# Kernel optimization log

Hardware: AMD Instinct MI355X
Metric: run time of the kernel (lower is better)

## Reference

```python
import jax, jax.numpy as jnp
import numpy as np

STRIDES = (8, 4, 2, 1)
EPS = 1e-12  # F.normalize default eps


def _l2norm(x):
    return x / jnp.maximum(jnp.linalg.norm(x, axis=-1, keepdims=True), EPS)


def _stage(residual, stride, iw, ib, ow, ob, cb):
    B, D, T = residual.shape
    # avg_pool1d(stride, stride)
    zp = residual.reshape(B, D, T // stride, stride).mean(-1) if stride > 1 else residual
    # in_proj: 1x1 conv  [B,D,Ts] -> [B,C,Ts]
    z_e = jnp.einsum('bdt,cd->bct', zp, iw) + ib[None, :, None]
    C = z_e.shape[1]
    enc = z_e.transpose(0, 2, 1).reshape(-1, C)           # (B*Ts, C)
    enc_n = _l2norm(enc)
    cb_n = _l2norm(cb)
    dist = (enc_n ** 2).sum(1, keepdims=True) - 2.0 * enc_n @ cb_n.T + (cb_n ** 2).sum(1)[None, :]
    indices = jnp.argmax(-dist, axis=1).reshape(B, -1)    # (B, Ts)
    z_q = cb[indices].transpose(0, 2, 1)                  # (B, C, Ts) -- unnormalized codebook lookup
    commit = ((z_e - jax.lax.stop_gradient(z_q)) ** 2).mean(axis=(1, 2))
    cbloss = ((z_q - jax.lax.stop_gradient(z_e)) ** 2).mean(axis=(1, 2))
    z_q = z_e + jax.lax.stop_gradient(z_q - z_e)          # straight-through
    z_q_out = jnp.einsum('bct,dc->bdt', z_q, ow) + ob[None, :, None]
    if stride > 1:
        z_q_out = jnp.repeat(z_q_out, stride, axis=-1)
        z_e = jnp.repeat(z_e, stride, axis=-1)
    return z_q_out, commit, cbloss, indices, z_e


def setup_inputs() -> dict:
    key = jax.random.key(0)
    ks = jax.random.split(key, 6)
    return {
        'z': jax.random.normal(ks[0], (16, 512, 4096), dtype=jnp.float32),
        'in_w': jax.random.normal(ks[1], (4, 8, 512), dtype=jnp.float32) * 0.05,
        'in_b': jax.random.normal(ks[2], (4, 8), dtype=jnp.float32) * 0.05,
        'out_w': jax.random.normal(ks[3], (4, 512, 8), dtype=jnp.float32) * 0.05,
        'out_b': jax.random.normal(ks[4], (4, 512), dtype=jnp.float32) * 0.05,
        'codebooks': jax.random.normal(ks[5], (4, 1024, 8), dtype=jnp.float32),
    }


def reference(z, in_w, in_b, out_w, out_b, codebooks):
    z_q = jnp.zeros_like(z)
    residual = z
    commitment_loss = 0.0
    codebook_loss = 0.0
    codes = []
    latents = []
    for i, s in enumerate(STRIDES):
        z_q_i, commit_i, cbloss_i, idx_i, z_e_i = _stage(
            residual, s, in_w[i], in_b[i], out_w[i], out_b[i], codebooks[i])
        z_q = z_q + z_q_i  # mask is all-True in eval with n_quantizers = n_codebooks
        residual = residual - z_q_i
        commitment_loss = commitment_loss + commit_i.mean()
        codebook_loss = codebook_loss + cbloss_i.mean()
        codes.append(idx_i)
        latents.append(z_e_i)
    latents = jnp.concatenate(latents, axis=1)  # [B, N*C, T]
    return (z_q, latents, commitment_loss, codebook_loss,
            codes[0], codes[1], codes[2], codes[3])
```

## Files before the change

kernel.cpp:

```cpp
#include <hip/hip_runtime.h>


constexpr int B = 16, D = 512, T = 4096, C = 8, K = 1024, NS = 4;

constexpr long long OUT_ZQ     = 0;
constexpr long long OUT_LAT    = 33554432LL;
constexpr long long OUT_COMMIT = OUT_LAT + 2097152LL;
constexpr long long OUT_CBL    = OUT_COMMIT + 1;
constexpr long long OUT_CODES0 = OUT_CBL + 1;

__host__ __device__ constexpr long long code_off(int j) {
    return OUT_CODES0 + (j >= 1 ? 8192 : 0) + (j >= 2 ? 16384 : 0) + (j >= 3 ? 32768 : 0);
}

constexpr long long WS_CBREC = 0;
constexpr long long WS_OBS   = 49152;
constexpr long long WS_LOSS  = 49664;
constexpr long long WS_CORR  = 49696;
constexpr long long WS_P0    = 52224;
constexpr long long WS_P1    = WS_P0 + 65536;
constexpr long long WS_P2    = WS_P1 + 131072;
constexpr long long WS_P3    = WS_P2 + 262144;
constexpr long long WS_Q0    = WS_P3 + 524288;
constexpr long long WS_Q1    = WS_Q0 + 65536;
constexpr long long WS_Q2    = WS_Q1 + 131072;
constexpr long long WS_Q3    = WS_Q2 + 262144;
constexpr long long WS_TAB   = WS_Q3 + 524288;

__global__ __launch_bounds__(256) void k_prep(
    const float* __restrict__ in_w, const float* __restrict__ out_w,
    const float* __restrict__ out_b, const float* __restrict__ cb,
    float* __restrict__ ws)
{
    int bid = blockIdx.x;
    int tid = threadIdx.x;

    if (bid < 18) {
        int t = bid * 256 + tid;
        if (t == 0) ws[WS_LOSS] = 0.f;
        if (t < NS * K) {
            const float* c = cb + (long long)t * 8;
            float cv[8];
#pragma unroll
            for (int k = 0; k < 8; k++) cv[k] = c[k];
            float n2 = 0.f;
#pragma unroll
            for (int k = 0; k < 8; k++) n2 += cv[k] * cv[k];
            float den = fmaxf(sqrtf(n2), 1e-12f);
            float cn[8];
#pragma unroll
            for (int k = 0; k < 8; k++) cn[k] = cv[k] / den;
            float cn2 = 0.f;
#pragma unroll
            for (int k = 0; k < 8; k++) cn2 += cn[k] * cn[k];
            float* r = ws + WS_CBREC + (long long)t * 12;
#pragma unroll
            for (int k = 0; k < 8; k++) r[k] = -2.0f * cn[k];
            r[8] = cn2; r[9] = 0.f; r[10] = 0.f; r[11] = 0.f;
        } else if (t < NS * K + D) {
            int d = t - NS * K;
            ws[WS_OBS + d] = out_b[d] + out_b[512 + d] + out_b[1024 + d] + out_b[1536 + d];
        }
        return;
    }

    int gw = (bid - 18) * 4 + (tid >> 6);
    int lane = tid & 63;
    if (gw >= 6 * 72) return;
    int p = gw / 72, idx = gw % 72;
    int i, j;
    if (p == 0) { i = 1; j = 0; }
    else if (p < 3) { i = 2; j = p - 1; }
    else { i = 3; j = p - 3; }

    double acc = 0.0;
    if (idx < 64) {
        int ci = idx >> 3, cc = idx & 7;
        const float* wi = in_w + (long long)(i * 8 + ci) * 512;
        const float* wo = out_w + (long long)j * 4096;
#pragma unroll
        for (int k = 0; k < 8; k++) {
            int d = lane + k * 64;
            acc += (double)wi[d] * (double)wo[d * 8 + cc];
        }
    } else {
        int ci = idx - 64;
        const float* wi = in_w + (long long)(i * 8 + ci) * 512;
        const float* bo = out_b + (long long)j * 512;
#pragma unroll
        for (int k = 0; k < 8; k++) {
            int d = lane + k * 64;
            acc += (double)wi[d] * (double)bo[d];
        }
    }
#pragma unroll
    for (int off = 32; off >= 1; off >>= 1) acc += __shfl_down(acc, off);
    if (lane == 0) ((double*)(ws + WS_CORR))[p * 72 + idx] = acc;
}

__global__ __launch_bounds__(256) void k_prep_c(
    const float* __restrict__ cb, float* __restrict__ ws)
{
    int t = blockIdx.x * 256 + threadIdx.x;
    if (t >= 6 * 1024) return;
    int p = t >> 10, code = t & 1023;
    int j = (p == 0) ? 0 : (p < 3) ? (p - 1) : (p - 3);
    const double* M = (const double*)(ws + WS_CORR) + p * 72;
    const float* q = cb + ((long long)j * K + code) * 8;
    float qv[8];
#pragma unroll
    for (int cc = 0; cc < 8; cc++) qv[cc] = q[cc];
    float* trow = ws + WS_TAB + (long long)t * 8;
#pragma unroll
    for (int c = 0; c < 8; c++) {
        double acc = M[64 + c];
#pragma unroll
        for (int cc = 0; cc < 8; cc++) acc += M[c * 8 + cc] * (double)qv[cc];
        trow[c] = (float)acc;
    }
}

__global__ __launch_bounds__(512) void k_pool_proj(
    const float* __restrict__ z, const float* __restrict__ in_w,
    const float* __restrict__ in_b, float* __restrict__ ws)
{
    __shared__ float smem[512 * 36];

    int tid = threadIdx.x;
    int lane = tid & 63;
    int wv = __builtin_amdgcn_readfirstlane(tid >> 6);
    int b = blockIdx.x;
    int t0 = blockIdx.y * 128;

#pragma unroll
    for (int sc = 0; sc < 32; ++sc)
        smem[tid * 36 + sc] = in_w[sc * 512 + tid];
    __syncthreads();

    const float* zrow = z + ((long long)b * D) * T + t0 + lane * 2;

    float a3[2][8] = {};
    float a2[8]    = {};
    float a1[8]    = {};
    float a0[8]    = {};

#pragma unroll 2
    for (int dd = 0; dd < 64; dd++) {
        int d = wv * 64 + dd;
        float2 v = *(const float2*)(zrow + (long long)d * T);
        const float* wrow = smem + d * 36;
        float w0[8], w1[8], w2[8], w3[8];
        *(float4*)&w0[0] = *(const float4*)(wrow + 0);
        *(float4*)&w0[4] = *(const float4*)(wrow + 4);
        *(float4*)&w1[0] = *(const float4*)(wrow + 8);
        *(float4*)&w1[4] = *(const float4*)(wrow + 12);
        *(float4*)&w2[0] = *(const float4*)(wrow + 16);
        *(float4*)&w2[4] = *(const float4*)(wrow + 20);
        *(float4*)&w3[0] = *(const float4*)(wrow + 24);
        *(float4*)&w3[4] = *(const float4*)(wrow + 28);

        float s2 = v.x + v.y;
#pragma unroll
        for (int c = 0; c < 8; c++) {
            a3[0][c] = fmaf(w3[c], v.x, a3[0][c]);
            a3[1][c] = fmaf(w3[c], v.y, a3[1][c]);
            a2[c]    = fmaf(w2[c], s2, a2[c]);
            a1[c]    = fmaf(w1[c], s2, a1[c]);
            a0[c]    = fmaf(w0[c], s2, a0[c]);
        }
    }

    __syncthreads();

    {
        float (*red)[16][64] = (float (*)[16][64])smem;
#pragma unroll
        for (int pos = 0; pos < 2; pos++)
#pragma unroll
            for (int c = 0; c < 8; c++)
                red[wv][pos * 8 + c][lane] = a3[pos][c];
        __syncthreads();
        for (int o = tid; o < 1024; o += 512) {
            int ln = o & 63, s = o >> 6;
            float sum = 0.f;
#pragma unroll
            for (int w = 0; w < 8; w++) sum += red[w][s][ln];
            int pos = s >> 3, c = s & 7;
            int tp = t0 + ln * 2 + pos;
            ws[WS_P3 + ((long long)b * 4096 + tp) * 8 + c] = sum + in_b[3 * 8 + c];
        }
        __syncthreads();
    }

    {
        float (*red)[24][64] = (float (*)[24][64])smem;
#pragma unroll
        for (int c = 0; c < 8; c++) {
            red[wv][c][lane]      = a2[c];
            red[wv][8 + c][lane]  = a1[c];
            red[wv][16 + c][lane] = a0[c];
        }
        __syncthreads();
        for (int o = tid; o < 1536; o += 512) {
            int ln = o & 63, s = o >> 6;
            if (s < 8) {
                int c = s;
                float sum = 0.f;
#pragma unroll
                for (int w = 0; w < 8; w++) sum += red[w][s][ln];
                int tp = (t0 >> 1) + ln;
                ws[WS_P2 + ((long long)b * 2048 + tp) * 8 + c] = sum * 0.5f + in_b[2 * 8 + c];
            } else if (s < 16) {
                if (ln >= 32) continue;
                int c = s - 8;
                float sum = 0.f;
#pragma unroll
                for (int w = 0; w < 8; w++) sum += red[w][s][2 * ln] + red[w][s][2 * ln + 1];
                int tp = (t0 >> 2) + ln;
                ws[WS_P1 + ((long long)b * 1024 + tp) * 8 + c] = sum * 0.25f + in_b[8 + c];
            } else {
                if (ln >= 16) continue;
                int c = s - 16;
                float sum = 0.f;
#pragma unroll
                for (int w = 0; w < 8; w++)
#pragma unroll
                    for (int k = 0; k < 4; k++) sum += red[w][s][4 * ln + k];
                int tp = (t0 >> 3) + ln;
                ws[WS_P0 + ((long long)b * 512 + tp) * 8 + c] = sum * 0.125f + in_b[c];
            }
        }
    }
}

template <int S>
__global__ __launch_bounds__(512) void k_vq(
    const float* __restrict__ cb, float* __restrict__ ws, float* __restrict__ out)
{
    constexpr int TS = 512 << S;
    constexpr long long PBASE = (S == 0) ? WS_P0 : (S == 1) ? WS_P1 : (S == 2) ? WS_P2 : WS_P3;
    constexpr long long QBASE = (S == 0) ? WS_Q0 : (S == 1) ? WS_Q1 : (S == 2) ? WS_Q2 : WS_Q3;
    constexpr int pbase = (S == 1) ? 0 : (S == 2) ? 1 : 3;
    constexpr float LW = 1.0f / (8.0f * (float)TS * (float)B);

    __shared__ float cbl[12288];
    __shared__ float sb[8][64];
    __shared__ unsigned short si[8][64];
    __shared__ float e_lds[64][8];

    int tid = threadIdx.x;
    int lane = tid & 63;
    int w = __builtin_amdgcn_readfirstlane(tid >> 6);

    {
        const float4* src = (const float4*)(ws + WS_CBREC + (long long)S * K * 12);
        float4* dst = (float4*)cbl;
        for (int o = tid; o < 3072; o += 512) dst[o] = src[o];
    }

    long long v = (long long)blockIdx.x * 64 + lane;
    int b = (int)(v >> (9 + S));
    int tp = (int)(v & (TS - 1));

    float e[8];
    const float* P = ws + PBASE + v * 8;
#pragma unroll
    for (int c = 0; c < 8; c++) e[c] = P[c];

    if (S > 0) {
        double ed[8];
#pragma unroll
        for (int c = 0; c < 8; c++) ed[c] = (double)e[c];
#pragma unroll
        for (int j = 0; j < S; j++) {
            int tj = tp >> (S - j);
            long long vj = ((long long)b << (9 + j)) + tj;
            int cidx = (int)out[code_off(j) + vj];
            const float* trow = ws + WS_TAB + ((long long)(pbase + j) * 1024 + cidx) * 8;
#pragma unroll
            for (int c = 0; c < 8; c++) ed[c] -= (double)trow[c];
        }
#pragma unroll
        for (int c = 0; c < 8; c++) e[c] = (float)ed[c];
    }

    float n2 = 0.f;
#pragma unroll
    for (int c = 0; c < 8; c++) n2 = fmaf(e[c], e[c], n2);
    float den = fmaxf(sqrtf(n2), 1e-12f);
    float inv = 1.0f / den;
    float en[8];
#pragma unroll
    for (int c = 0; c < 8; c++) en[c] = e[c] * inv;

    if (w == 0) {
#pragma unroll
        for (int c = 0; c < 8; c++) e_lds[lane][c] = e[c];
    }

    __syncthreads();

    const float* rec = cbl + w * 128 * 12;
    float best = 3.0e38f;
    int bidx = 0;
    for (int jt = 0; jt < 128; jt++) {
        const float* r = rec + jt * 12;
        float acc = r[8];
#pragma unroll
        for (int c = 0; c < 8; c++) acc = fmaf(r[c], en[c], acc);
        if (acc < best) { best = acc; bidx = jt; }
    }
    sb[w][lane] = best;
    si[w][lane] = (unsigned short)(w * 128 + bidx);
    __syncthreads();

    if (tid < 64) {
        float bd = sb[0][lane];
        int bj = si[0][lane];
#pragma unroll
        for (int ww = 1; ww < 8; ww++) {
            float d2 = sb[ww][lane];
            int j2 = si[ww][lane];
            if (d2 < bd || (d2 == bd && j2 < bj)) { bd = d2; bj = j2; }
        }
        const float* qc = cb + ((long long)S * K + bj) * 8;
        float qv[8];
#pragma unroll
        for (int c = 0; c < 8; c++) qv[c] = qc[c];
        float* qo = ws + QBASE + v * 8;
#pragma unroll
        for (int c = 0; c < 8; c++) qo[c] = qv[c];

        out[code_off(S) + v] = (float)bj;

        float l = 0.f;
#pragma unroll
        for (int c = 0; c < 8; c++) { float dq = e[c] - qv[c]; l = fmaf(dq, dq, l); }
#pragma unroll
        for (int off = 32; off >= 1; off >>= 1) l += __shfl_down(l, off);
        if (lane == 0) atomicAdd(ws + WS_LOSS, l * LW);
    }

    constexpr int SREP = 8 >> S;
    {
        long long v0 = (long long)blockIdx.x * 64;
        int b0 = (int)(v0 >> (9 + S));
        int tp0 = (int)(v0 & (TS - 1));
        long long lat0 = OUT_LAT + ((long long)b0 * 32 + S * 8) * T + (long long)tp0 * SREP;
        for (int o = tid; o < 512 * SREP; o += 512) {
            int c = o / (64 * SREP);
            int r = o & (64 * SREP - 1);
            out[lat0 + (long long)c * T + r] = e_lds[r / SREP][c];
        }
    }
}

__global__ __launch_bounds__(256) void k_zq(
    const float* __restrict__ out_w, const float* __restrict__ ws, float* __restrict__ out)
{
    int tid = threadIdx.x;
    int lane = tid & 63;
    int w = __builtin_amdgcn_readfirstlane(tid >> 6);
    int bid = blockIdx.x;
    int tc   = bid & 3;
    int g    = (bid >> 2) & 63;
    int b    = bid >> 8;
    int t    = tc * 1024 + w * 256 + lane * 4;

    float q0[8], q1[8], q2[2][8], q3[4][8];
    {
        const float* Q = ws + WS_Q0 + ((long long)b * 512 + (t >> 3)) * 8;
#pragma unroll
        for (int c = 0; c < 8; c++) q0[c] = Q[c];
    }
    {
        const float* Q = ws + WS_Q1 + ((long long)b * 1024 + (t >> 2)) * 8;
#pragma unroll
        for (int c = 0; c < 8; c++) q1[c] = Q[c];
    }
    {
        const float* Q = ws + WS_Q2 + ((long long)b * 2048 + (t >> 1)) * 8;
#pragma unroll
        for (int j = 0; j < 2; j++)
#pragma unroll
            for (int c = 0; c < 8; c++) q2[j][c] = Q[j * 8 + c];
    }
    {
        const float* Q = ws + WS_Q3 + ((long long)b * 4096 + t) * 8;
#pragma unroll
        for (int j = 0; j < 4; j++)
#pragma unroll
            for (int c = 0; c < 8; c++) q3[j][c] = Q[j * 8 + c];
    }

#pragma unroll 2
    for (int dl = 0; dl < 8; dl++) {
        int d = g * 8 + dl;
        const float* w0 = out_w + 0 * 4096 + d * 8;
        const float* w1 = out_w + 1 * 4096 + d * 8;
        const float* w2 = out_w + 2 * 4096 + d * 8;
        const float* w3 = out_w + 3 * 4096 + d * 8;

        float acc = ws[WS_OBS + d];
#pragma unroll
        for (int c = 0; c < 8; c++) acc = fmaf(w0[c], q0[c], acc);
#pragma unroll
        for (int c = 0; c < 8; c++) acc = fmaf(w1[c], q1[c], acc);
        float accA = acc, accB = acc;
#pragma unroll
        for (int c = 0; c < 8; c++) {
            accA = fmaf(w2[c], q2[0][c], accA);
            accB = fmaf(w2[c], q2[1][c], accB);
        }
        float r0 = accA, r1 = accA, r2 = accB, r3 = accB;
#pragma unroll
        for (int c = 0; c < 8; c++) {
            r0 = fmaf(w3[c], q3[0][c], r0);
            r1 = fmaf(w3[c], q3[1][c], r1);
            r2 = fmaf(w3[c], q3[2][c], r2);
            r3 = fmaf(w3[c], q3[3][c], r3);
        }
        float* o = out + OUT_ZQ + ((long long)b * 512 + d) * T + t;
        *(float4*)o = make_float4(r0, r1, r2, r3);
    }

    if (bid == 0 && tid == 0) {
        float L = ws[WS_LOSS];
        out[OUT_COMMIT] = L;
        out[OUT_CBL]    = L;
    }
}

extern "C" void kernel_launch(void* const* d_in, const int* in_sizes, int n_in,
                              void* d_out, int out_size, void* d_ws, size_t ws_size,
                              hipStream_t stream)
{
    const float* z     = (const float*)d_in[0];
    const float* in_w  = (const float*)d_in[1];
    const float* in_b  = (const float*)d_in[2];
    const float* out_w = (const float*)d_in[3];
    const float* out_b = (const float*)d_in[4];
    const float* cb    = (const float*)d_in[5];
    float* out = (float*)d_out;
    float* ws  = (float*)d_ws;

    k_prep<<<dim3(126), dim3(256), 0, stream>>>(in_w, out_w, out_b, cb, ws);
    k_prep_c<<<dim3(24), dim3(256), 0, stream>>>(cb, ws);
    k_pool_proj<<<dim3(16, 32), dim3(512), 0, stream>>>(z, in_w, in_b, ws);
    k_vq<0><<<dim3(128), dim3(512), 0, stream>>>(cb, ws, out);
    k_vq<1><<<dim3(256), dim3(512), 0, stream>>>(cb, ws, out);
    k_vq<2><<<dim3(512), dim3(512), 0, stream>>>(cb, ws, out);
    k_vq<3><<<dim3(1024), dim3(512), 0, stream>>>(cb, ws, out);
    k_zq<<<dim3(4096), dim3(256), 0, stream>>>(out_w, ws, out);
}
```

Baseline: 151.1 us.

## Fuse prep kernels into pool/vq launches, process two vectors per thread in VQ

Merges the codebook/correction prep work into extra blocks of the pool-projection kernel and moves the table-building prep into the stage-0 VQ kernel, cutting two launches. Each VQ thread now scores two vectors per codebook record, halving the block count and reusing each LDS record read. It also adds software prefetch of z rows in the pooling loop and float4 latent stores. The cost is more registers per VQ thread and reuse of the codebook LDS buffer for the argmin reduction.

```diff
diff --git a/kernel.cpp b/kernel.cpp
--- a/kernel.cpp
+++ b/kernel.cpp
@@ -27,110 +27,84 @@
 constexpr long long WS_Q3    = WS_Q2 + 262144;
 constexpr long long WS_TAB   = WS_Q3 + 524288;
 
-__global__ __launch_bounds__(256) void k_prep(
-    const float* __restrict__ in_w, const float* __restrict__ out_w,
+__global__ __launch_bounds__(512) void k_pool_prep(
+    const float* __restrict__ z, const float* __restrict__ in_w,
+    const float* __restrict__ in_b, const float* __restrict__ out_w,
     const float* __restrict__ out_b, const float* __restrict__ cb,
     float* __restrict__ ws)
 {
+    __shared__ float smem[512 * 36];
+
     int bid = blockIdx.x;
     int tid = threadIdx.x;
-
-    if (bid < 18) {
-        int t = bid * 256 + tid;
-        if (t == 0) ws[WS_LOSS] = 0.f;
-        if (t < NS * K) {
-            const float* c = cb + (long long)t * 8;
-            float cv[8];
-#pragma unroll
-            for (int k = 0; k < 8; k++) cv[k] = c[k];
-            float n2 = 0.f;
-#pragma unroll
-            for (int k = 0; k < 8; k++) n2 += cv[k] * cv[k];
-            float den = fmaxf(sqrtf(n2), 1e-12f);
-            float cn[8];
-#pragma unroll
-            for (int k = 0; k < 8; k++) cn[k] = cv[k] / den;
-            float cn2 = 0.f;
-#pragma unroll
-            for (int k = 0; k < 8; k++) cn2 += cn[k] * cn[k];
-            float* r = ws + WS_CBREC + (long long)t * 12;
-#pragma unroll
-            for (int k = 0; k < 8; k++) r[k] = -2.0f * cn[k];
-            r[8] = cn2; r[9] = 0.f; r[10] = 0.f; r[11] = 0.f;
-        } else if (t < NS * K + D) {
-            int d = t - NS * K;
-            ws[WS_OBS + d] = out_b[d] + out_b[512 + d] + out_b[1024 + d] + out_b[1536 + d];
+    int lane = tid & 63;
+
+    if (bid >= 512) {
+        if (bid < 521) {
+            int t = (bid - 512) * 512 + tid;
+            if (t == 0) ws[WS_LOSS] = 0.f;
+            if (t < NS * K) {
+                const float* c = cb + (long long)t * 8;
+                float cv[8];
+#pragma unroll
+                for (int k = 0; k < 8; k++) cv[k] = c[k];
+                float n2 = 0.f;
+#pragma unroll
+                for (int k = 0; k < 8; k++) n2 += cv[k] * cv[k];
+                float den = fmaxf(sqrtf(n2), 1e-12f);
+                float cn[8];
+#pragma unroll
+                for (int k = 0; k < 8; k++) cn[k] = cv[k] / den;
+                float cn2 = 0.f;
+#pragma unroll
+                for (int k = 0; k < 8; k++) cn2 += cn[k] * cn[k];
+                float* r = ws + WS_CBREC + (long long)t * 12;
+#pragma unroll
+                for (int k = 0; k < 8; k++) r[k] = -2.0f * cn[k];
+                r[8] = cn2; r[9] = 0.f; r[10] = 0.f; r[11] = 0.f;
+            } else if (t < NS * K + D) {
+                int d = t - NS * K;
+                ws[WS_OBS + d] = out_b[d] + out_b[512 + d] + out_b[1024 + d] + out_b[1536 + d];
+            }
+        } else {
+            int gw = (bid - 521) * 8 + (tid >> 6);
+            if (gw >= 6 * 72) return;
+            int p = gw / 72, idx = gw % 72;
+            int i, j;
+            if (p == 0) { i = 1; j = 0; }
+            else if (p < 3) { i = 2; j = p - 1; }
+            else { i = 3; j = p - 3; }
+
+            double acc = 0.0;
+            if (idx < 64) {
+                int ci = idx >> 3, cc = idx & 7;
+                const float* wi = in_w + (long long)(i * 8 + ci) * 512;
+                const float* wo = out_w + (long long)j * 4096;
+#pragma unroll
+                for (int k = 0; k < 8; k++) {
+                    int d = lane + k * 64;
+                    acc += (double)wi[d] * (double)wo[d * 8 + cc];
+                }
+            } else {
+                int ci = idx - 64;
+                const float* wi = in_w + (long long)(i * 8 + ci) * 512;
+                const float* bo = out_b + (long long)j * 512;
+#pragma unroll
+                for (int k = 0; k < 8; k++) {
+                    int d = lane + k * 64;
+                    acc += (double)wi[d] * (double)bo[d];
+                }
+            }
+#pragma unroll
+            for (int off = 32; off >= 1; off >>= 1) acc += __shfl_down(acc, off);
+            if (lane == 0) ((double*)(ws + WS_CORR))[p * 72 + idx] = acc;
         }
         return;
     }
 
-    int gw = (bid - 18) * 4 + (tid >> 6);
-    int lane = tid & 63;
-    if (gw >= 6 * 72) return;
-    int p = gw / 72, idx = gw % 72;
-    int i, j;
-    if (p == 0) { i = 1; j = 0; }
-    else if (p < 3) { i = 2; j = p - 1; }
-    else { i = 3; j = p - 3; }
-
-    double acc = 0.0;
-    if (idx < 64) {
-        int ci = idx >> 3, cc = idx & 7;
-        const float* wi = in_w + (long long)(i * 8 + ci) * 512;
-        const float* wo = out_w + (long long)j * 4096;
-#pragma unroll
-        for (int k = 0; k < 8; k++) {
-            int d = lane + k * 64;
-            acc += (double)wi[d] * (double)wo[d * 8 + cc];
-        }
-    } else {
-        int ci = idx - 64;
-        const float* wi = in_w + (long long)(i * 8 + ci) * 512;
-        const float* bo = out_b + (long long)j * 512;
-#pragma unroll
-        for (int k = 0; k < 8; k++) {
-            int d = lane + k * 64;
-            acc += (double)wi[d] * (double)bo[d];
-        }
-    }
-#pragma unroll
-    for (int off = 32; off >= 1; off >>= 1) acc += __shfl_down(acc, off);
-    if (lane == 0) ((double*)(ws + WS_CORR))[p * 72 + idx] = acc;
-}
-
-__global__ __launch_bounds__(256) void k_prep_c(
-    const float* __restrict__ cb, float* __restrict__ ws)
-{
-    int t = blockIdx.x * 256 + threadIdx.x;
-    if (t >= 6 * 1024) return;
-    int p = t >> 10, code = t & 1023;
-    int j = (p == 0) ? 0 : (p < 3) ? (p - 1) : (p - 3);
-    const double* M = (const double*)(ws + WS_CORR) + p * 72;
-    const float* q = cb + ((long long)j * K + code) * 8;
-    float qv[8];
-#pragma unroll
-    for (int cc = 0; cc < 8; cc++) qv[cc] = q[cc];
-    float* trow = ws + WS_TAB + (long long)t * 8;
-#pragma unroll
-    for (int c = 0; c < 8; c++) {
-        double acc = M[64 + c];
-#pragma unroll
-        for (int cc = 0; cc < 8; cc++) acc += M[c * 8 + cc] * (double)qv[cc];
-        trow[c] = (float)acc;
-    }
-}
-
-__global__ __launch_bounds__(512) void k_pool_proj(
-    const float* __restrict__ z, const float* __restrict__ in_w,
-    const float* __restrict__ in_b, float* __restrict__ ws)
-{
-    __shared__ float smem[512 * 36];
-
-    int tid = threadIdx.x;
-    int lane = tid & 63;
     int wv = __builtin_amdgcn_readfirstlane(tid >> 6);
-    int b = blockIdx.x;
-    int t0 = blockIdx.y * 128;
+    int b = bid & 15;
+    int t0 = (bid >> 4) * 128;
 
 #pragma unroll
     for (int sc = 0; sc < 32; ++sc)
@@ -144,10 +118,17 @@
     float a1[8]    = {};
     float a0[8]    = {};
 
+    float2 zv0 = *(const float2*)(zrow + (long long)(wv * 64 + 0) * T);
+    float2 zv1 = *(const float2*)(zrow + (long long)(wv * 64 + 1) * T);
+
 #pragma unroll 2
     for (int dd = 0; dd < 64; dd++) {
         int d = wv * 64 + dd;
-        float2 v = *(const float2*)(zrow + (long long)d * T);
+        float2 v = zv0;
+        zv0 = zv1;
+        if (dd < 62)
+            zv1 = *(const float2*)(zrow + (long long)(d + 2) * T);
+
         const float* wrow = smem + d * 36;
         float w0[8], w1[8], w2[8], w3[8];
         *(float4*)&w0[0] = *(const float4*)(wrow + 0);
@@ -244,13 +225,12 @@
     constexpr float LW = 1.0f / (8.0f * (float)TS * (float)B);
 
     __shared__ float cbl[12288];
-    __shared__ float sb[8][64];
-    __shared__ unsigned short si[8][64];
-    __shared__ float e_lds[64][8];
+    __shared__ float e_lds[128][8];
 
     int tid = threadIdx.x;
     int lane = tid & 63;
     int w = __builtin_amdgcn_readfirstlane(tid >> 6);
+    int bid = blockIdx.x;
 
     {
         const float4* src = (const float4*)(ws + WS_CBREC + (long long)S * K * 12);
@@ -258,71 +238,89 @@
         for (int o = tid; o < 3072; o += 512) dst[o] = src[o];
     }
 
-    long long v = (long long)blockIdx.x * 64 + lane;
-    int b = (int)(v >> (9 + S));
-    int tp = (int)(v & (TS - 1));
-
-    float e[8];
-    const float* P = ws + PBASE + v * 8;
-#pragma unroll
-    for (int c = 0; c < 8; c++) e[c] = P[c];
-
-    if (S > 0) {
-        double ed[8];
-#pragma unroll
-        for (int c = 0; c < 8; c++) ed[c] = (double)e[c];
-#pragma unroll
-        for (int j = 0; j < S; j++) {
-            int tj = tp >> (S - j);
-            long long vj = ((long long)b << (9 + j)) + tj;
-            int cidx = (int)out[code_off(j) + vj];
-            const float* trow = ws + WS_TAB + ((long long)(pbase + j) * 1024 + cidx) * 8;
-#pragma unroll
-            for (int c = 0; c < 8; c++) ed[c] -= (double)trow[c];
-        }
-#pragma unroll
-        for (int c = 0; c < 8; c++) e[c] = (float)ed[c];
-    }
-
-    float n2 = 0.f;
-#pragma unroll
-    for (int c = 0; c < 8; c++) n2 = fmaf(e[c], e[c], n2);
-    float den = fmaxf(sqrtf(n2), 1e-12f);
-    float inv = 1.0f / den;
-    float en[8];
-#pragma unroll
-    for (int c = 0; c < 8; c++) en[c] = e[c] * inv;
-
-    if (w == 0) {
-#pragma unroll
-        for (int c = 0; c < 8; c++) e_lds[lane][c] = e[c];
+    float enA[8], enB[8];
+    {
+        long long vv[2] = { (long long)bid * 128 + lane, (long long)bid * 128 + 64 + lane };
+#pragma unroll
+        for (int h = 0; h < 2; h++) {
+            long long v = vv[h];
+            int b = (int)(v >> (9 + S));
+            int tp = (int)(v & (TS - 1));
+            float e[8];
+            const float* P = ws + PBASE + v * 8;
+#pragma unroll
+            for (int c = 0; c < 8; c++) e[c] = P[c];
+            if (S > 0) {
+                double ed[8];
+#pragma unroll
+                for (int c = 0; c < 8; c++) ed[c] = (double)e[c];
+#pragma unroll
+                for (int j = 0; j < S; j++) {
+                    int tj = tp >> (S - j);
+                    long long vj = ((long long)b << (9 + j)) + tj;
+                    int cidx = (int)out[code_off(j) + vj];
+                    const float* trow = ws + WS_TAB + ((long long)(pbase + j) * 1024 + cidx) * 8;
+#pragma unroll
+                    for (int c = 0; c < 8; c++) ed[c] -= (double)trow[c];
+                }
+#pragma unroll
+                for (int c = 0; c < 8; c++) e[c] = (float)ed[c];
+            }
+            float n2 = 0.f;
+#pragma unroll
+            for (int c = 0; c < 8; c++) n2 = fmaf(e[c], e[c], n2);
+            float den = fmaxf(sqrtf(n2), 1e-12f);
+            float inv = 1.0f / den;
+            float* en = h ? enB : enA;
+#pragma unroll
+            for (int c = 0; c < 8; c++) en[c] = e[c] * inv;
+            if (w == 0) {
+#pragma unroll
+                for (int c = 0; c < 8; c++) e_lds[h * 64 + lane][c] = e[c];
+            }
+        }
     }
 
     __syncthreads();
 
     const float* rec = cbl + w * 128 * 12;
-    float best = 3.0e38f;
-    int bidx = 0;
+    float bestA = 3.0e38f, bestB = 3.0e38f;
+    int idxA = 0, idxB = 0;
+#pragma unroll 2
     for (int jt = 0; jt < 128; jt++) {
         const float* r = rec + jt * 12;
-        float acc = r[8];
-#pragma unroll
-        for (int c = 0; c < 8; c++) acc = fmaf(r[c], en[c], acc);
-        if (acc < best) { best = acc; bidx = jt; }
-    }
-    sb[w][lane] = best;
-    si[w][lane] = (unsigned short)(w * 128 + bidx);
+        float aA = r[8], aB = r[8];
+#pragma unroll
+        for (int c = 0; c < 8; c++) {
+            float rc = r[c];
+            aA = fmaf(rc, enA[c], aA);
+            aB = fmaf(rc, enB[c], aB);
+        }
+        if (aA < bestA) { bestA = aA; idxA = jt; }
+        if (aB < bestB) { bestB = aB; idxB = jt; }
+    }
+
     __syncthreads();
 
-    if (tid < 64) {
-        float bd = sb[0][lane];
-        int bj = si[0][lane];
+    float* sb_f = cbl;
+    unsigned short* si_u = (unsigned short*)(cbl + 1024);
+    sb_f[w * 128 + lane]      = bestA;
+    sb_f[w * 128 + 64 + lane] = bestB;
+    si_u[w * 128 + lane]      = (unsigned short)(w * 128 + idxA);
+    si_u[w * 128 + 64 + lane] = (unsigned short)(w * 128 + idxB);
+    __syncthreads();
+
+    if (tid < 128) {
+        int sv = tid;
+        float bd = sb_f[sv];
+        int bj = si_u[sv];
 #pragma unroll
         for (int ww = 1; ww < 8; ww++) {
-            float d2 = sb[ww][lane];
-            int j2 = si[ww][lane];
+            float d2 = sb_f[ww * 128 + sv];
+            int j2 = si_u[ww * 128 + sv];
             if (d2 < bd || (d2 == bd && j2 < bj)) { bd = d2; bj = j2; }
         }
+        long long v = (long long)bid * 128 + sv;
         const float* qc = cb + ((long long)S * K + bj) * 8;
         float qv[8];
 #pragma unroll
@@ -335,22 +333,50 @@
 
         float l = 0.f;
 #pragma unroll
-        for (int c = 0; c < 8; c++) { float dq = e[c] - qv[c]; l = fmaf(dq, dq, l); }
+        for (int c = 0; c < 8; c++) { float dq = e_lds[sv][c] - qv[c]; l = fmaf(dq, dq, l); }
 #pragma unroll
         for (int off = 32; off >= 1; off >>= 1) l += __shfl_down(l, off);
-        if (lane == 0) atomicAdd(ws + WS_LOSS, l * LW);
+        if ((tid & 63) == 0) atomicAdd(ws + WS_LOSS, l * LW);
     }
 
     constexpr int SREP = 8 >> S;
-    {
-        long long v0 = (long long)blockIdx.x * 64;
+    constexpr int SH = 3 - S;
+    {
+        long long v0 = (long long)bid * 128;
         int b0 = (int)(v0 >> (9 + S));
         int tp0 = (int)(v0 & (TS - 1));
         long long lat0 = OUT_LAT + ((long long)b0 * 32 + S * 8) * T + (long long)tp0 * SREP;
-        for (int o = tid; o < 512 * SREP; o += 512) {
-            int c = o / (64 * SREP);
-            int r = o & (64 * SREP - 1);
-            out[lat0 + (long long)c * T + r] = e_lds[r / SREP][c];
+        for (int o = tid; o < 256 * SREP; o += 512) {
+            int c = o / (32 * SREP);
+            int i4 = o % (32 * SREP);
+            int r0 = i4 * 4;
+            float4 vv = make_float4(
+                e_lds[(r0 + 0) >> SH][c], e_lds[(r0 + 1) >> SH][c],
+                e_lds[(r0 + 2) >> SH][c], e_lds[(r0 + 3) >> SH][c]);
+            *(float4*)(out + lat0 + (long long)c * T + r0) = vv;
+        }
+    }
+
+    if constexpr (S == 0) {
+        if (bid < 12) {
+            int t = bid * 512 + tid;
+            if (t < 6 * 1024) {
+                int p = t >> 10, code = t & 1023;
+                int j = (p == 0) ? 0 : (p < 3) ? (p - 1) : (p - 3);
+                const double* M = (const double*)(ws + WS_CORR) + p * 72;
+                const float* q = cb + ((long long)j * K + code) * 8;
+                float qvv[8];
+#pragma unroll
+                for (int cc = 0; cc < 8; cc++) qvv[cc] = q[cc];
+                float* trow = ws + WS_TAB + (long long)t * 8;
+#pragma unroll
+                for (int c = 0; c < 8; c++) {
+                    double acc = M[64 + c];
+#pragma unroll
+                    for (int cc = 0; cc < 8; cc++) acc += M[c * 8 + cc] * (double)qvv[cc];
+                    trow[c] = (float)acc;
+                }
+            }
         }
     }
 }
@@ -444,12 +470,10 @@
     float* out = (float*)d_out;
     float* ws  = (float*)d_ws;
 
-    k_prep<<<dim3(126), dim3(256), 0, stream>>>(in_w, out_w, out_b, cb, ws);
-    k_prep_c<<<dim3(24), dim3(256), 0, stream>>>(cb, ws);
-    k_pool_proj<<<dim3(16, 32), dim3(512), 0, stream>>>(z, in_w, in_b, ws);
-    k_vq<0><<<dim3(128), dim3(512), 0, stream>>>(cb, ws, out);
-    k_vq<1><<<dim3(256), dim3(512), 0, stream>>>(cb, ws, out);
-    k_vq<2><<<dim3(512), dim3(512), 0, stream>>>(cb, ws, out);
-    k_vq<3><<<dim3(1024), dim3(512), 0, stream>>>(cb, ws, out);
+    k_pool_prep<<<dim3(575), dim3(512), 0, stream>>>(z, in_w, in_b, out_w, out_b, cb, ws);
+    k_vq<0><<<dim3(64),  dim3(512), 0, stream>>>(cb, ws, out);
+    k_vq<1><<<dim3(128), dim3(512), 0, stream>>>(cb, ws, out);
+    k_vq<2><<<dim3(256), dim3(512), 0, stream>>>(cb, ws, out);
+    k_vq<3><<<dim3(512), dim3(512), 0, stream>>>(cb, ws, out);
     k_zq<<<dim3(4096), dim3(256), 0, stream>>>(out_w, ws, out);
 }
```

After: 169.3 us. 1.12x slower.

## Register-block VQ search over four vectors, widen pool tiles, fold prep_c into pool

Applied to the files above, without the earlier changes.

Each VQ thread now scores four encoder vectors per codebook entry, so every loaded codebook row is reused four times. The codebook is stored as a packed 8-float record plus a separate norm array, and latents are written as float4. The pooling/projection kernel handles 256 time steps per block with float4 loads. The k_prep_c table computation becomes an extra grid row of k_pool_proj, which removes one launch. The trade-off is fewer VQ blocks (as few as 32 for stage 0) and higher register pressure, which may leave the GPU underfilled.

```diff
diff --git a/kernel.cpp b/kernel.cpp
--- a/kernel.cpp
+++ b/kernel.cpp
@@ -14,10 +14,11 @@
 }
 
 constexpr long long WS_CBREC = 0;
-constexpr long long WS_OBS   = 49152;
-constexpr long long WS_LOSS  = 49664;
-constexpr long long WS_CORR  = 49696;
-constexpr long long WS_P0    = 52224;
+constexpr long long WS_CN2   = 32768;
+constexpr long long WS_OBS   = 36864;
+constexpr long long WS_LOSS  = 37376;
+constexpr long long WS_CORR  = 37384;
+constexpr long long WS_P0    = 40960;
 constexpr long long WS_P1    = WS_P0 + 65536;
 constexpr long long WS_P2    = WS_P1 + 131072;
 constexpr long long WS_P3    = WS_P2 + 262144;
@@ -52,11 +53,11 @@
             for (int k = 0; k < 8; k++) cn[k] = cv[k] / den;
             float cn2 = 0.f;
 #pragma unroll
-            for (int k = 0; k < 8; k++) cn2 += cn[k] * cn[k];
-            float* r = ws + WS_CBREC + (long long)t * 12;
+            for (int k = 0; k < 8; k++) cn2 = fmaf(cn[k], cn[k], cn2);
+            float* r = ws + WS_CBREC + (long long)t * 8;
 #pragma unroll
             for (int k = 0; k < 8; k++) r[k] = -2.0f * cn[k];
-            r[8] = cn2; r[9] = 0.f; r[10] = 0.f; r[11] = 0.f;
+            ws[WS_CN2 + t] = cn2;
         } else if (t < NS * K + D) {
             int d = t - NS * K;
             ws[WS_OBS + d] = out_b[d] + out_b[512 + d] + out_b[1024 + d] + out_b[1536 + d];
@@ -98,56 +99,58 @@
     if (lane == 0) ((double*)(ws + WS_CORR))[p * 72 + idx] = acc;
 }
 
-__global__ __launch_bounds__(256) void k_prep_c(
-    const float* __restrict__ cb, float* __restrict__ ws)
-{
-    int t = blockIdx.x * 256 + threadIdx.x;
-    if (t >= 6 * 1024) return;
-    int p = t >> 10, code = t & 1023;
-    int j = (p == 0) ? 0 : (p < 3) ? (p - 1) : (p - 3);
-    const double* M = (const double*)(ws + WS_CORR) + p * 72;
-    const float* q = cb + ((long long)j * K + code) * 8;
-    float qv[8];
-#pragma unroll
-    for (int cc = 0; cc < 8; cc++) qv[cc] = q[cc];
-    float* trow = ws + WS_TAB + (long long)t * 8;
-#pragma unroll
-    for (int c = 0; c < 8; c++) {
-        double acc = M[64 + c];
-#pragma unroll
-        for (int cc = 0; cc < 8; cc++) acc += M[c * 8 + cc] * (double)qv[cc];
-        trow[c] = (float)acc;
-    }
-}
-
 __global__ __launch_bounds__(512) void k_pool_proj(
     const float* __restrict__ z, const float* __restrict__ in_w,
-    const float* __restrict__ in_b, float* __restrict__ ws)
+    const float* __restrict__ in_b, const float* __restrict__ cb,
+    float* __restrict__ ws)
 {
     __shared__ float smem[512 * 36];
 
     int tid = threadIdx.x;
     int lane = tid & 63;
+
+    if (blockIdx.y == 16) {
+        int t = blockIdx.x * 512 + tid;
+        if (t < 6 * 1024) {
+            int p = t >> 10, code = t & 1023;
+            int j = (p == 0) ? 0 : (p < 3) ? (p - 1) : (p - 3);
+            const double* M = (const double*)(ws + WS_CORR) + p * 72;
+            const float* q = cb + ((long long)j * K + code) * 8;
+            float qv[8];
+#pragma unroll
+            for (int cc = 0; cc < 8; cc++) qv[cc] = q[cc];
+            float* trow = ws + WS_TAB + (long long)t * 8;
+#pragma unroll
+            for (int c = 0; c < 8; c++) {
+                double acc = M[64 + c];
+#pragma unroll
+                for (int cc = 0; cc < 8; cc++) acc += M[c * 8 + cc] * (double)qv[cc];
+                trow[c] = (float)acc;
+            }
+        }
+        return;
+    }
+
     int wv = __builtin_amdgcn_readfirstlane(tid >> 6);
     int b = blockIdx.x;
-    int t0 = blockIdx.y * 128;
+    int t0 = blockIdx.y * 256;
 
 #pragma unroll
     for (int sc = 0; sc < 32; ++sc)
         smem[tid * 36 + sc] = in_w[sc * 512 + tid];
     __syncthreads();
 
-    const float* zrow = z + ((long long)b * D) * T + t0 + lane * 2;
-
-    float a3[2][8] = {};
-    float a2[8]    = {};
+    const float* zrow = z + ((long long)b * D) * T + t0 + lane * 4;
+
+    float a3[4][8] = {};
+    float a2[2][8] = {};
     float a1[8]    = {};
     float a0[8]    = {};
 
 #pragma unroll 2
     for (int dd = 0; dd < 64; dd++) {
         int d = wv * 64 + dd;
-        float2 v = *(const float2*)(zrow + (long long)d * T);
+        float4 v = *(const float4*)(zrow + (long long)d * T);
         const float* wrow = smem + d * 36;
         float w0[8], w1[8], w2[8], w3[8];
         *(float4*)&w0[0] = *(const float4*)(wrow + 0);
@@ -159,74 +162,79 @@
         *(float4*)&w3[0] = *(const float4*)(wrow + 24);
         *(float4*)&w3[4] = *(const float4*)(wrow + 28);
 
-        float s2 = v.x + v.y;
+        float s2a = v.x + v.y, s2b = v.z + v.w;
+        float s4 = s2a + s2b;
 #pragma unroll
         for (int c = 0; c < 8; c++) {
             a3[0][c] = fmaf(w3[c], v.x, a3[0][c]);
             a3[1][c] = fmaf(w3[c], v.y, a3[1][c]);
-            a2[c]    = fmaf(w2[c], s2, a2[c]);
-            a1[c]    = fmaf(w1[c], s2, a1[c]);
-            a0[c]    = fmaf(w0[c], s2, a0[c]);
+            a3[2][c] = fmaf(w3[c], v.z, a3[2][c]);
+            a3[3][c] = fmaf(w3[c], v.w, a3[3][c]);
+            a2[0][c] = fmaf(w2[c], s2a, a2[0][c]);
+            a2[1][c] = fmaf(w2[c], s2b, a2[1][c]);
+            a1[c]    = fmaf(w1[c], s4, a1[c]);
+            a0[c]    = fmaf(w0[c], s4, a0[c]);
         }
     }
 
     __syncthreads();
 
     {
-        float (*red)[16][64] = (float (*)[16][64])smem;
-#pragma unroll
-        for (int pos = 0; pos < 2; pos++)
+        float (*red)[32][64] = (float (*)[32][64])smem;
+#pragma unroll
+        for (int pos = 0; pos < 4; pos++)
 #pragma unroll
             for (int c = 0; c < 8; c++)
                 red[wv][pos * 8 + c][lane] = a3[pos][c];
         __syncthreads();
-        for (int o = tid; o < 1024; o += 512) {
+        for (int o = tid; o < 2048; o += 512) {
             int ln = o & 63, s = o >> 6;
             float sum = 0.f;
 #pragma unroll
             for (int w = 0; w < 8; w++) sum += red[w][s][ln];
             int pos = s >> 3, c = s & 7;
-            int tp = t0 + ln * 2 + pos;
+            int tp = t0 + ln * 4 + pos;
             ws[WS_P3 + ((long long)b * 4096 + tp) * 8 + c] = sum + in_b[3 * 8 + c];
         }
         __syncthreads();
     }
 
     {
-        float (*red)[24][64] = (float (*)[24][64])smem;
+        float (*red)[32][64] = (float (*)[32][64])smem;
+#pragma unroll
+        for (int pos = 0; pos < 2; pos++)
+#pragma unroll
+            for (int c = 0; c < 8; c++)
+                red[wv][pos * 8 + c][lane] = a2[pos][c];
 #pragma unroll
         for (int c = 0; c < 8; c++) {
-            red[wv][c][lane]      = a2[c];
-            red[wv][8 + c][lane]  = a1[c];
-            red[wv][16 + c][lane] = a0[c];
+            red[wv][16 + c][lane] = a1[c];
+            red[wv][24 + c][lane] = a0[c];
         }
         __syncthreads();
-        for (int o = tid; o < 1536; o += 512) {
+        for (int o = tid; o < 2048; o += 512) {
             int ln = o & 63, s = o >> 6;
-            if (s < 8) {
-                int c = s;
+            if (s < 16) {
                 float sum = 0.f;
 #pragma unroll
                 for (int w = 0; w < 8; w++) sum += red[w][s][ln];
-                int tp = (t0 >> 1) + ln;
+                int pos = s >> 3, c = s & 7;
+                int tp = (t0 >> 1) + ln * 2 + pos;
                 ws[WS_P2 + ((long long)b * 2048 + tp) * 8 + c] = sum * 0.5f + in_b[2 * 8 + c];
-            } else if (s < 16) {
-                if (ln >= 32) continue;
-                int c = s - 8;
+            } else if (s < 24) {
+                int c = s - 16;
                 float sum = 0.f;
 #pragma unroll
-                for (int w = 0; w < 8; w++) sum += red[w][s][2 * ln] + red[w][s][2 * ln + 1];
+                for (int w = 0; w < 8; w++) sum += red[w][s][ln];
                 int tp = (t0 >> 2) + ln;
                 ws[WS_P1 + ((long long)b * 1024 + tp) * 8 + c] = sum * 0.25f + in_b[8 + c];
             } else {
-                if (ln >= 16) continue;
-                int c = s - 16;
+                if (ln & 1) continue;
+                int c = s - 24;
                 float sum = 0.f;
 #pragma unroll
-                for (int w = 0; w < 8; w++)
-#pragma unroll
-                    for (int k = 0; k < 4; k++) sum += red[w][s][4 * ln + k];
-                int tp = (t0 >> 3) + ln;
+                for (int w = 0; w < 8; w++) sum += red[w][s][ln] + red[w][s][ln + 1];
+                int tp = (t0 >> 3) + (ln >> 1);
                 ws[WS_P0 + ((long long)b * 512 + tp) * 8 + c] = sum * 0.125f + in_b[c];
             }
         }
@@ -243,86 +251,120 @@
     constexpr int pbase = (S == 1) ? 0 : (S == 2) ? 1 : 3;
     constexpr float LW = 1.0f / (8.0f * (float)TS * (float)B);
 
-    __shared__ float cbl[12288];
-    __shared__ float sb[8][64];
-    __shared__ unsigned short si[8][64];
-    __shared__ float e_lds[64][8];
+    __shared__ float recl[1024 * 8];
+    __shared__ float cn2l[1024];
+    __shared__ float e_lds[256][8];
+    __shared__ float sbl[8][256];
+    __shared__ unsigned short sil[8][256];
 
     int tid = threadIdx.x;
     int lane = tid & 63;
     int w = __builtin_amdgcn_readfirstlane(tid >> 6);
-
-    {
-        const float4* src = (const float4*)(ws + WS_CBREC + (long long)S * K * 12);
-        float4* dst = (float4*)cbl;
-        for (int o = tid; o < 3072; o += 512) dst[o] = src[o];
-    }
-
-    long long v = (long long)blockIdx.x * 64 + lane;
-    int b = (int)(v >> (9 + S));
-    int tp = (int)(v & (TS - 1));
-
-    float e[8];
-    const float* P = ws + PBASE + v * 8;
-#pragma unroll
-    for (int c = 0; c < 8; c++) e[c] = P[c];
-
-    if (S > 0) {
-        double ed[8];
-#pragma unroll
-        for (int c = 0; c < 8; c++) ed[c] = (double)e[c];
-#pragma unroll
-        for (int j = 0; j < S; j++) {
-            int tj = tp >> (S - j);
-            long long vj = ((long long)b << (9 + j)) + tj;
-            int cidx = (int)out[code_off(j) + vj];
-            const float* trow = ws + WS_TAB + ((long long)(pbase + j) * 1024 + cidx) * 8;
-#pragma unroll
-            for (int c = 0; c < 8; c++) ed[c] -= (double)trow[c];
-        }
-#pragma unroll
-        for (int c = 0; c < 8; c++) e[c] = (float)ed[c];
-    }
-
-    float n2 = 0.f;
-#pragma unroll
-    for (int c = 0; c < 8; c++) n2 = fmaf(e[c], e[c], n2);
-    float den = fmaxf(sqrtf(n2), 1e-12f);
-    float inv = 1.0f / den;
-    float en[8];
-#pragma unroll
-    for (int c = 0; c < 8; c++) en[c] = e[c] * inv;
-
-    if (w == 0) {
-#pragma unroll
-        for (int c = 0; c < 8; c++) e_lds[lane][c] = e[c];
+    int bid = blockIdx.x;
+
+    {
+        const float4* rs = (const float4*)(ws + WS_CBREC + (long long)S * 8192);
+        float4* rd = (float4*)recl;
+        for (int o = tid; o < 2048; o += 512) rd[o] = rs[o];
+        const float4* cs = (const float4*)(ws + WS_CN2 + (long long)S * 1024);
+        float4* cd = (float4*)cn2l;
+        for (int o = tid; o < 256; o += 512) cd[o] = cs[o];
+    }
+
+    float en[4][8];
+#pragma unroll
+    for (int h = 0; h < 4; h++) {
+        int sv = h * 64 + lane;
+        long long v = (long long)bid * 256 + sv;
+        int b = (int)(v >> (9 + S));
+        int tp = (int)(v & (TS - 1));
+
+        float e[8];
+        const float* P = ws + PBASE + v * 8;
+#pragma unroll
+        for (int c = 0; c < 8; c++) e[c] = P[c];
+
+        if constexpr (S > 0) {
+            double ed[8];
+#pragma unroll
+            for (int c = 0; c < 8; c++) ed[c] = (double)e[c];
+#pragma unroll
+            for (int j = 0; j < S; j++) {
+                int tj = tp >> (S - j);
+                long long vj = ((long long)b << (9 + j)) + tj;
+                int cidx = (int)out[code_off(j) + vj];
+                const float* trow = ws + WS_TAB + ((long long)(pbase + j) * 1024 + cidx) * 8;
+#pragma unroll
+                for (int c = 0; c < 8; c++) ed[c] -= (double)trow[c];
+            }
+#pragma unroll
+            for (int c = 0; c < 8; c++) e[c] = (float)ed[c];
+        }
+
+        float n2 = 0.f;
+#pragma unroll
+        for (int c = 0; c < 8; c++) n2 = fmaf(e[c], e[c], n2);
+        float den = fmaxf(sqrtf(n2), 1e-12f);
+        float inv = 1.0f / den;
+#pragma unroll
+        for (int c = 0; c < 8; c++) en[h][c] = e[c] * inv;
+        if (w == 0) {
+#pragma unroll
+            for (int c = 0; c < 8; c++) e_lds[sv][c] = e[c];
+        }
     }
 
     __syncthreads();
 
-    const float* rec = cbl + w * 128 * 12;
-    float best = 3.0e38f;
-    int bidx = 0;
-    for (int jt = 0; jt < 128; jt++) {
-        const float* r = rec + jt * 12;
-        float acc = r[8];
-#pragma unroll
-        for (int c = 0; c < 8; c++) acc = fmaf(r[c], en[c], acc);
-        if (acc < best) { best = acc; bidx = jt; }
-    }
-    sb[w][lane] = best;
-    si[w][lane] = (unsigned short)(w * 128 + bidx);
+    const float* rec = recl + w * 128 * 8;
+    const float* c2  = cn2l + w * 128;
+    float best0 = 3.0e38f, best1 = 3.0e38f, best2 = 3.0e38f, best3 = 3.0e38f;
+    int bi0 = 0, bi1 = 0, bi2 = 0, bi3 = 0;
+
+    for (int j0 = 0; j0 < 128; j0 += 4) {
+        float4 cq = *(const float4*)(c2 + j0);
+        float cqa[4] = { cq.x, cq.y, cq.z, cq.w };
+#pragma unroll
+        for (int k = 0; k < 4; k++) {
+            int jt = j0 + k;
+            const float* r = rec + jt * 8;
+            float rr[8];
+            *(float4*)&rr[0] = *(const float4*)(r + 0);
+            *(float4*)&rr[4] = *(const float4*)(r + 4);
+            float cc = cqa[k];
+            float a0 = cc, a1 = cc, a2 = cc, a3 = cc;
+#pragma unroll
+            for (int c = 0; c < 8; c++) {
+                float rc = rr[c];
+                a0 = fmaf(rc, en[0][c], a0);
+                a1 = fmaf(rc, en[1][c], a1);
+                a2 = fmaf(rc, en[2][c], a2);
+                a3 = fmaf(rc, en[3][c], a3);
+            }
+            if (a0 < best0) { best0 = a0; bi0 = jt; }
+            if (a1 < best1) { best1 = a1; bi1 = jt; }
+            if (a2 < best2) { best2 = a2; bi2 = jt; }
+            if (a3 < best3) { best3 = a3; bi3 = jt; }
+        }
+    }
+
+    sbl[w][lane]       = best0;  sil[w][lane]       = (unsigned short)(w * 128 + bi0);
+    sbl[w][64 + lane]  = best1;  sil[w][64 + lane]  = (unsigned short)(w * 128 + bi1);
+    sbl[w][128 + lane] = best2;  sil[w][128 + lane] = (unsigned short)(w * 128 + bi2);
+    sbl[w][192 + lane] = best3;  sil[w][192 + lane] = (unsigned short)(w * 128 + bi3);
     __syncthreads();
 
-    if (tid < 64) {
-        float bd = sb[0][lane];
-        int bj = si[0][lane];
+    if (tid < 256) {
+        int sv = tid;
+        float bd = sbl[0][sv];
+        int bj = sil[0][sv];
 #pragma unroll
         for (int ww = 1; ww < 8; ww++) {
-            float d2 = sb[ww][lane];
-            int j2 = si[ww][lane];
+            float d2 = sbl[ww][sv];
+            int j2 = sil[ww][sv];
             if (d2 < bd || (d2 == bd && j2 < bj)) { bd = d2; bj = j2; }
         }
+        long long v = (long long)bid * 256 + sv;
         const float* qc = cb + ((long long)S * K + bj) * 8;
         float qv[8];
 #pragma unroll
@@ -335,22 +377,27 @@
 
         float l = 0.f;
 #pragma unroll
-        for (int c = 0; c < 8; c++) { float dq = e[c] - qv[c]; l = fmaf(dq, dq, l); }
+        for (int c = 0; c < 8; c++) { float dq = e_lds[sv][c] - qv[c]; l = fmaf(dq, dq, l); }
 #pragma unroll
         for (int off = 32; off >= 1; off >>= 1) l += __shfl_down(l, off);
-        if (lane == 0) atomicAdd(ws + WS_LOSS, l * LW);
+        if ((tid & 63) == 0) atomicAdd(ws + WS_LOSS, l * LW);
     }
 
     constexpr int SREP = 8 >> S;
-    {
-        long long v0 = (long long)blockIdx.x * 64;
+    constexpr int SH = 3 - S;
+    {
+        long long v0 = (long long)bid * 256;
         int b0 = (int)(v0 >> (9 + S));
         int tp0 = (int)(v0 & (TS - 1));
         long long lat0 = OUT_LAT + ((long long)b0 * 32 + S * 8) * T + (long long)tp0 * SREP;
         for (int o = tid; o < 512 * SREP; o += 512) {
             int c = o / (64 * SREP);
-            int r = o & (64 * SREP - 1);
-            out[lat0 + (long long)c * T + r] = e_lds[r / SREP][c];
+            int i4 = o % (64 * SREP);
+            int r0 = i4 * 4;
+            float4 vv = make_float4(
+                e_lds[(r0 + 0) >> SH][c], e_lds[(r0 + 1) >> SH][c],
+                e_lds[(r0 + 2) >> SH][c], e_lds[(r0 + 3) >> SH][c]);
+            *(float4*)(out + lat0 + (long long)c * T + r0) = vv;
         }
     }
 }
@@ -445,11 +492,10 @@
     float* ws  = (float*)d_ws;
 
     k_prep<<<dim3(126), dim3(256), 0, stream>>>(in_w, out_w, out_b, cb, ws);
-    k_prep_c<<<dim3(24), dim3(256), 0, stream>>>(cb, ws);
-    k_pool_proj<<<dim3(16, 32), dim3(512), 0, stream>>>(z, in_w, in_b, ws);
-    k_vq<0><<<dim3(128), dim3(512), 0, stream>>>(cb, ws, out);
-    k_vq<1><<<dim3(256), dim3(512), 0, stream>>>(cb, ws, out);
-    k_vq<2><<<dim3(512), dim3(512), 0, stream>>>(cb, ws, out);
-    k_vq<3><<<dim3(1024), dim3(512), 0, stream>>>(cb, ws, out);
+    k_pool_proj<<<dim3(16, 17), dim3(512), 0, stream>>>(z, in_w, in_b, cb, ws);
+    k_vq<0><<<dim3(32),  dim3(512), 0, stream>>>(cb, ws, out);
+    k_vq<1><<<dim3(64),  dim3(512), 0, stream>>>(cb, ws, out);
+    k_vq<2><<<dim3(128), dim3(512), 0, stream>>>(cb, ws, out);
+    k_vq<3><<<dim3(256), dim3(512), 0, stream>>>(cb, ws, out);
     k_zq<<<dim3(4096), dim3(256), 0, stream>>>(out_w, ws, out);
 }
```

After: 186.1 us. 23.2% more time.
